# Optimization experiments

Measured on AMD Instinct MI355X. Metric: run time of the kernel, lower is better.

## Reference

```python
import jax, jax.numpy as jnp
import numpy as np

LN_EPS = 1e-5
EPSILON = 1e-8
NUM_ITERS = 3
SLOT_SIZE = 128
NUM_SLOTS = 7
MLP_HIDDEN = 256


def _layernorm(x, g, b):
    m = jnp.mean(x, axis=-1, keepdims=True)
    v = jnp.var(x, axis=-1, keepdims=True)
    return (x - m) * jax.lax.rsqrt(v + LN_EPS) * g + b


def setup_inputs() -> dict:
    key = jax.random.key(0)
    ks = jax.random.split(key, 16)
    B, N, D, S, H, M = 64, 4096, 128, NUM_SLOTS, SLOT_SIZE, MLP_HIDDEN
    sc = 0.05
    return {
        "inputs": jax.random.normal(ks[0], (B, N, D), jnp.float32),
        "slots_init": jax.random.normal(ks[1], (B, S, H + 4), jnp.float32),
        "ln_in_g": jnp.ones((D,), jnp.float32), "ln_in_b": jnp.zeros((D,), jnp.float32),
        "ln_s_g": jnp.ones((H,), jnp.float32), "ln_s_b": jnp.zeros((H,), jnp.float32),
        "ln_m_g": jnp.ones((H,), jnp.float32), "ln_m_b": jnp.zeros((H,), jnp.float32),
        "Wq": jax.random.normal(ks[2], (H, H), jnp.float32) * sc,
        "Wk": jax.random.normal(ks[3], (H, H), jnp.float32) * sc,
        "Wv": jax.random.normal(ks[4], (H, H), jnp.float32) * sc,
        "W_ih": jax.random.normal(ks[5], (3 * H, H), jnp.float32) * sc,
        "W_hh": jax.random.normal(ks[6], (3 * H, H), jnp.float32) * sc,
        "b_ih": jnp.zeros((3 * H,), jnp.float32),
        "b_hh": jnp.zeros((3 * H,), jnp.float32),
        "mlp_w1": jax.random.normal(ks[7], (M, H), jnp.float32) * sc,
        "mlp_b1": jnp.zeros((M,), jnp.float32),
        "mlp_w2": jax.random.normal(ks[8], (H, M), jnp.float32) * sc,
        "mlp_b2": jnp.zeros((H,), jnp.float32),
        "slots_mu": jax.random.normal(ks[9], (1, 1, H + 4), jnp.float32) * sc,
        "slots_log_sigma": jax.random.normal(ks[10], (1, 1, H + 4), jnp.float32) * sc,
    }


def _gru_cell(x, h, W_ih, W_hh, b_ih, b_hh):
    # torch.nn.GRUCell math; x, h: [..., H]
    gi = x @ W_ih.T + b_ih
    gh = h @ W_hh.T + b_hh
    i_r, i_z, i_n = jnp.split(gi, 3, axis=-1)
    h_r, h_z, h_n = jnp.split(gh, 3, axis=-1)
    r = jax.nn.sigmoid(i_r + h_r)
    z = jax.nn.sigmoid(i_z + h_z)
    n = jnp.tanh(i_n + r * h_n)
    return (1.0 - z) * n + z * h


def reference(inputs, slots_init, ln_in_g, ln_in_b, ln_s_g, ln_s_b, ln_m_g, ln_m_b,
              Wq, Wk, Wv, W_ih, W_hh, b_ih, b_hh, mlp_w1, mlp_b1, mlp_w2, mlp_b2,
              slots_mu, slots_log_sigma):
    x = _layernorm(inputs, ln_in_g, ln_in_b)           # [B, N, D]
    k = x @ Wk.T                                       # [B, N, H]
    v = x @ Wv.T                                       # [B, N, H]
    slots_full = slots_mu + jnp.exp(slots_log_sigma) * slots_init  # [B, S, H+4]
    slots = slots_full[..., :SLOT_SIZE]                # positions/scales discarded
    scale = SLOT_SIZE ** -0.5
    for _ in range(NUM_ITERS):
        slots_prev = slots
        sn = _layernorm(slots, ln_s_g, ln_s_b)
        q = sn @ Wq.T                                  # [B, S, H]
        logits = scale * jnp.einsum('bnh,bsh->bns', k, q)
        attn = jax.nn.softmax(logits, axis=-1) + EPSILON
        attn = attn / jnp.sum(attn, axis=1, keepdims=True)
        updates = jnp.einsum('bns,bnh->bsh', attn, v)  # [B, S, H]
        slots = _gru_cell(updates, slots_prev, W_ih, W_hh, b_ih, b_hh)
        slots = slots + (jax.nn.relu(_layernorm(slots, ln_m_g, ln_m_b) @ mlp_w1.T + mlp_b1) @ mlp_w2.T + mlp_b2)
    return slots
```

## Files before the change

kernel.cpp:

```cpp
#include <hip/hip_runtime.h>
#include <hip/hip_bf16.h>
#include <stdint.h>

typedef unsigned int u32;
typedef unsigned short u16;
typedef float v2f __attribute__((ext_vector_type(2)));
typedef short bf16x8 __attribute__((ext_vector_type(8)));
typedef float f32x4 __attribute__((ext_vector_type(4)));

#define LN_EPS_ 1e-5f
#define EPS_ 1e-8f

__device__ __forceinline__ float bflo(u32 v){ return __uint_as_float(v << 16); }
__device__ __forceinline__ float bfhi(u32 v){ return __uint_as_float(v & 0xFFFF0000u); }
__device__ __forceinline__ u32 f2bf(float f){
    u32 x = __float_as_uint(f);
    return (x + 0x7FFFu + ((x >> 16) & 1u)) >> 16;
}
__device__ __forceinline__ u32 pack2bf(float a, float b){
    union { __hip_bfloat162 h; u32 u; } cv;
    cv.h = __float22bfloat162_rn(float2{a, b});
    return cv.u;
}
__device__ __forceinline__ v2f pkfma(v2f a, v2f b, v2f c){
    v2f d; asm("v_pk_fma_f32 %0, %1, %2, %3" : "=v"(d) : "v"(a), "v"(b), "v"(c)); return d;
}
__device__ __forceinline__ v2f pkadd(v2f a, v2f b){
    v2f d; asm("v_pk_add_f32 %0, %1, %2" : "=v"(d) : "v"(a), "v"(b)); return d;
}
__device__ __forceinline__ bf16x8 as_bf16x8(uint4 u){
    union { uint4 a; bf16x8 b; } c; c.a = u; return c.b;
}

__global__ __launch_bounds__(256) void k_pack(
    const float* __restrict__ Wq, const float* __restrict__ Wv,
    const float* __restrict__ Wih, const float* __restrict__ Whh,
    const float* __restrict__ w1, const float* __restrict__ w2,
    float* __restrict__ WqT, u32* __restrict__ Pv, u32* __restrict__ Pih,
    u32* __restrict__ Phh, u32* __restrict__ Pw1, u32* __restrict__ Pw2,
    u32* __restrict__ Rg32)
{
    int i = blockIdx.x * 256 + threadIdx.x;
    if (i < 8192) {
        int dp = i >> 7, o = i & 127;
        Pv[i] = pack2bf(Wv[o * 128 + 2 * dp], Wv[o * 128 + 2 * dp + 1]);
    } else if (i < 32768) {
        int r = i - 8192; int dp = r / 384, j = r - dp * 384;
        Pih[r] = pack2bf(Wih[j * 128 + 2 * dp], Wih[j * 128 + 2 * dp + 1]);
    } else if (i < 57344) {
        int r = i - 32768; int dp = r / 384, j = r - dp * 384;
        Phh[r] = pack2bf(Whh[j * 128 + 2 * dp], Whh[j * 128 + 2 * dp + 1]);
    } else if (i < 73728) {
        int r = i - 57344; int dp = r >> 8, j = r & 255;
        Pw1[r] = pack2bf(w1[j * 128 + 2 * dp], w1[j * 128 + 2 * dp + 1]);
    } else if (i < 90112) {
        int r = i - 73728; int mp = r >> 7, o = r & 127;
        Pw2[r] = pack2bf(w2[o * 256 + 2 * mp], w2[o * 256 + 2 * mp + 1]);
    } else if (i < 106496) {
        int r = i - 90112; int d = r >> 7, o = r & 127;
        WqT[r] = Wq[o * 128 + d];
    } else if (i < 143360) {
        int r = i - 106496; int b = r / 576, rem = r - b * 576;
        Rg32[b * 1024 + 448 + rem] = 0;
    }
}

__global__ __launch_bounds__(256) void k_init_prep(
    const float* __restrict__ slots_init, const float* __restrict__ mu,
    const float* __restrict__ ls, float* __restrict__ slots,
    const float* __restrict__ g_s, const float* __restrict__ b_s,
    const float* __restrict__ WqT, const float* __restrict__ Wk,
    const float* __restrict__ g_in, const float* __restrict__ b_in,
    u16* __restrict__ Rg, float* __restrict__ c1ws, float* __restrict__ c2ws)
{
    __shared__ float snb[128], qb[128], xch[128], red4[4];
    int bs = blockIdx.x, t = threadIdx.x;
    int b = bs / 7, s = bs - b * 7;
    int h = t & 127, half = t >> 7;
    float nv = 0.f;
    if (!half) {
        nv = mu[h] + expf(ls[h]) * slots_init[bs * 132 + h];
        slots[bs * 128 + h] = nv;
    }
    if (!half) {
        float smv = nv, sqv = nv * nv;
        for (int m = 32; m >= 1; m >>= 1) { smv += __shfl_xor(smv, m); sqv += __shfl_xor(sqv, m); }
        if ((t & 63) == 0) { red4[(t >> 6) * 2] = smv; red4[(t >> 6) * 2 + 1] = sqv; }
    }
    __syncthreads();
    float mean = (red4[0] + red4[2]) * (1.0f / 128.0f);
    float var  = (red4[1] + red4[3]) * (1.0f / 128.0f) - mean * mean;
    float rsv = rsqrtf(var + LN_EPS_);
    if (!half) snb[h] = (nv - mean) * rsv * g_s[h] + b_s[h];
    __syncthreads();
    {
        float q0 = 0.f, q1 = 0.f;
        int d0 = half * 64;
        #pragma unroll 4
        for (int d = d0; d < d0 + 64; d += 2) {
            q0 += WqT[d * 128 + h] * snb[d];
            q1 += WqT[(d + 1) * 128 + h] * snb[d + 1];
        }
        if (half) xch[h] = q0 + q1;
        __syncthreads();
        if (!half) qb[h] = q0 + q1 + xch[h];
        __syncthreads();
    }
    float r0 = 0.f, r1 = 0.f;
    int j0 = half * 64;
    #pragma unroll 4
    for (int j = j0; j < j0 + 64; j += 2) {
        r0 += Wk[j * 128 + h] * qb[j];
        r1 += Wk[(j + 1) * 128 + h] * qb[j + 1];
    }
    if (half) xch[h] = r0 + r1;
    __syncthreads();
    if (!half) {
        float r = (r0 + r1 + xch[h]) * 0.08838834764831845f;
        float rt  = g_in[h] * r;
        float c2v = b_in[h] * r;
        Rg[((size_t)b * 16 + s) * 128 + h] = (u16)f2bf(rt);
        float c1p = rt, c2p = c2v;
        for (int m = 32; m >= 1; m >>= 1) { c1p += __shfl_xor(c1p, m); c2p += __shfl_xor(c2p, m); }
        if ((t & 63) == 0) { red4[(t >> 6) * 2] = c1p; red4[(t >> 6) * 2 + 1] = c2p; }
    }
    __syncthreads();
    if (t == 0) {
        c1ws[b * 8 + s] = red4[0] + red4[2];
        c2ws[b * 8 + s] = red4[1] + red4[3];
    }
}

__global__ __launch_bounds__(256, 8) void k_attn(
    const float* __restrict__ xin,
    const u16* __restrict__ Rg, const float* __restrict__ c1ws,
    const float* __restrict__ c2ws,
    float* __restrict__ ypart, float* __restrict__ Zp, float* __restrict__ Ap)
{
    __shared__ u32 tile[4096];
    __shared__ __align__(16) float wt[448];
    __shared__ __align__(8)  float stats[128];
    __shared__ float c1l[16], c2l[16];
    __shared__ float redp[4][8], redw[4][8];
    int t = threadIdx.x;
    int b = blockIdx.y;
    int n0 = blockIdx.x * 64;
    int lane = t & 63, wv = t >> 6;
    int ls = lane & 15, lg = lane >> 4;
    size_t blk = (size_t)b * 64 + blockIdx.x;

    if (t < 16) {
        c1l[t] = (t < 7) ? c1ws[b * 8 + t] : 0.f;
        c2l[t] = (t < 7) ? c2ws[b * 8 + t] : 0.f;
    }

    bf16x8 bfr[4];
    {
        const u16* Rrow = Rg + ((size_t)b * 16 + ls) * 128;
        #pragma unroll
        for (int kk = 0; kk < 4; kk++)
            bfr[kk] = as_bf16x8(*(const uint4*)&Rrow[kk * 32 + lg * 8]);
    }

    {
        int r = t >> 2, p = t & 3;
        const float4* xg = (const float4*)(xin + ((size_t)b * 4096 + n0 + r) * 128 + p * 32);
        v2f smp = (v2f){0.f, 0.f}, sqp = (v2f){0.f, 0.f};
        #pragma unroll
        for (int i = 0; i < 8; i++) {
            float4 v = xg[i];
            v2f lo = (v2f){v.x, v.y}, hi = (v2f){v.z, v.w};
            smp = pkadd(smp, pkadd(lo, hi));
            sqp = pkfma(lo, lo, sqp);
            sqp = pkfma(hi, hi, sqp);
            int q = p * 4 + (i >> 1), rem = (i & 1) * 2;
            *(uint2*)&tile[(r * 16 + (q ^ (r & 15))) * 4 + rem] =
                make_uint2(pack2bf(v.x, v.y), pack2bf(v.z, v.w));
        }
        float sm = smp.x + smp.y, sq = sqp.x + sqp.y;
        sm += __shfl_xor(sm, 1); sq += __shfl_xor(sq, 1);
        sm += __shfl_xor(sm, 2); sq += __shfl_xor(sq, 2);
        if (!p) {
            float mean = sm * (1.0f / 128.0f);
            float var  = sq * (1.0f / 128.0f) - mean * mean;
            *(float2*)&stats[2 * r] = make_float2(mean, rsqrtf(var + LN_EPS_));
        }
    }
    __syncthreads();

    f32x4 acc0 = {0.f, 0.f, 0.f, 0.f};
    {
        int m0 = wv * 16 + ls;
        #pragma unroll
        for (int kk = 0; kk < 4; kk++) {
            int q = kk * 4 + lg;
            bf16x8 a0 = as_bf16x8(*(const uint4*)&tile[(m0 * 16 + (q ^ ls)) * 4]);
            acc0 = __builtin_amdgcn_mfma_f32_16x16x32_bf16(a0, bfr[kk], acc0, 0, 0, 0);
        }
    }
    {
        float zsum = 0.f, asum = 0.f;
        float c1v = c1l[ls], c2v = c2l[ls];
        bool sv = ls < 7;
        int nbase = wv * 16 + lg * 4;
        #pragma unroll
        for (int r4 = 0; r4 < 4; r4++) {
            int n = nbase + r4;
            float2 stf = *(const float2*)&stats[2 * n];
            float L = sv ? (stf.y * (acc0[r4] - stf.x * c1v) + c2v) : -3.4e38f;
            float mx = L;
            mx = fmaxf(mx, __shfl_xor(mx, 1));
            mx = fmaxf(mx, __shfl_xor(mx, 2));
            mx = fmaxf(mx, __shfl_xor(mx, 4));
            mx = fmaxf(mx, __shfl_xor(mx, 8));
            float e = __expf(L - mx);
            float ssum = e;
            ssum += __shfl_xor(ssum, 1);
            ssum += __shfl_xor(ssum, 2);
            ssum += __shfl_xor(ssum, 4);
            ssum += __shfl_xor(ssum, 8);
            float p = e * (1.0f / ssum) + EPS_;
            float w = p * stf.y;
            if (sv) {
                wt[ls * 64 + n] = w;
                zsum += p;
                asum += w * stf.x;
            }
        }
        zsum += __shfl_xor(zsum, 16); zsum += __shfl_xor(zsum, 32);
        asum += __shfl_xor(asum, 16); asum += __shfl_xor(asum, 32);
        if (lane < 7) { redp[wv][lane] = zsum; redw[wv][lane] = asum; }
    }
    __syncthreads();
    if (t < 7)
        Zp[blk * 8 + t] = redp[0][t] + redp[1][t] + redp[2][t] + redp[3][t];
    else if (t >= 64 && t < 71) {
        int s = t - 64;
        Ap[blk * 8 + s] = redw[0][s] + redw[1][s] + redw[2][s] + redw[3][s];
    }

    int nh = t >> 7, dp = t & 63, sA = (t >> 6) & 1;
    v2f aclo[4], achi[4];
    #pragma unroll
    for (int k = 0; k < 4; k++) { aclo[k] = (v2f){0.f,0.f}; achi[k] = (v2f){0.f,0.f}; }
    int nbeg = nh * 32;
    #pragma unroll 4
    for (int n = nbeg; n < nbeg + 32; n += 2) {
        u32 x0 = tile[(n * 16 + ((dp >> 2) ^ (n & 15))) * 4 + (dp & 3)];
        u32 x1 = tile[((n + 1) * 16 + ((dp >> 2) ^ ((n + 1) & 15))) * 4 + (dp & 3)];
        v2f alo = (v2f){bflo(x0), bflo(x1)};
        v2f ahi = (v2f){bfhi(x0), bfhi(x1)};
        #pragma unroll
        for (int k = 0; k < 4; k++) {
            int s = sA + 2 * k;
            if (s < 7) {
                v2f wp = *(const v2f*)&wt[s * 64 + n];
                aclo[k] = pkfma(alo, wp, aclo[k]);
                achi[k] = pkfma(ahi, wp, achi[k]);
            }
        }
    }
    float* ytmp = (float*)tile;
    __syncthreads();
    if (nh) {
        #pragma unroll
        for (int k = 0; k < 4; k++) {
            int s = sA + 2 * k;
            if (s < 7)
                *(float2*)&ytmp[s * 128 + 2 * dp] =
                    make_float2(aclo[k].x + aclo[k].y, achi[k].x + achi[k].y);
        }
    }
    __syncthreads();
    if (!nh) {
        float* yp = ypart + blk * 896;
        #pragma unroll
        for (int k = 0; k < 4; k++) {
            int s = sA + 2 * k;
            if (s < 7) {
                float2 o = *(const float2*)&ytmp[s * 128 + 2 * dp];
                *(float2*)&yp[s * 128 + 2 * dp] =
                    make_float2(aclo[k].x + aclo[k].y + o.x,
                                achi[k].x + achi[k].y + o.y);
            }
        }
    }
}

__global__ __launch_bounds__(512) void k_update(
    float* __restrict__ slots, const float* __restrict__ ypart,
    const float* __restrict__ Zp, const float* __restrict__ Ap,
    const float* __restrict__ g_in, const float* __restrict__ b_in,
    const u32* __restrict__ Pv, const u32* __restrict__ Pih,
    const u32* __restrict__ Phh, const float* __restrict__ b_ih,
    const float* __restrict__ b_hh, const float* __restrict__ g_m,
    const float* __restrict__ b_m, const u32* __restrict__ Pw1,
    const float* __restrict__ bb1, const u32* __restrict__ Pw2,
    const float* __restrict__ bb2, float* __restrict__ out,
    const float* __restrict__ g_s, const float* __restrict__ b_s,
    const float* __restrict__ WqT, const float* __restrict__ Wk,
    u16* __restrict__ Rg, float* __restrict__ c1ws, float* __restrict__ c2ws,
    int do_prep)
{
    __shared__ float ybuf[128], ub[128], hb[128], lb[128], t1b[256];
    __shared__ float red4w[4][128];
    __shared__ float g6[12][128];
    __shared__ float m1p[256];
    __shared__ float redA[2], redB[2];
    __shared__ float snb[128], qb[128], red4[4];
    __shared__ float Zsh, Ash;
    int bs = blockIdx.x, t = threadIdx.x;
    int b = bs / 7, s = bs - b * 7;
    int h = t & 127, q = t >> 7;
    {
        float ysum = 0.f;
        const float* bp = ypart + ((size_t)(b * 64 + q * 16)) * 896 + s * 128 + h;
        #pragma unroll 8
        for (int c = 0; c < 16; c++) ysum += bp[(size_t)c * 896];
        red4w[q][h] = ysum;
    }
    if (t < 64) {
        float z = Zp[((size_t)b * 64 + t) * 8 + s];
        for (int m = 32; m >= 1; m >>= 1) z += __shfl_xor(z, m);
        if (t == 0) Zsh = z;
    } else if (t < 128) {
        float a_ = Ap[((size_t)b * 64 + (t - 64)) * 8 + s];
        for (int m = 32; m >= 1; m >>= 1) a_ += __shfl_xor(a_, m);
        if (t == 64) Ash = a_;
    }
    __syncthreads();
    if (q == 0) {
        float ytot = red4w[0][h] + red4w[1][h] + red4w[2][h] + red4w[3][h];
        ybuf[h] = g_in[h] * (ytot - Ash) / Zsh + b_in[h];
        hb[h] = slots[bs * 128 + h];
    }
    __syncthreads();
    {
        float a0 = 0.f;
        int dp0 = q * 16;
        #pragma unroll 4
        for (int dp = dp0; dp < dp0 + 16; dp++) {
            u32 w0 = Pv[dp * 128 + h];
            a0 += bflo(w0) * ybuf[2 * dp] + bfhi(w0) * ybuf[2 * dp + 1];
        }
        red4w[q][h] = a0;
    }
    __syncthreads();
    if (q == 0) ub[h] = red4w[0][h] + red4w[1][h] + red4w[2][h] + red4w[3][h];
    __syncthreads();
    {
        const u32* P = (q >= 2) ? Phh : Pih;
        const float* src = (q >= 2) ? hb : ub;
        int dp0 = (q & 1) * 32;
        float gv0 = 0.f, gv1 = 0.f, gv2 = 0.f;
        #pragma unroll 4
        for (int dp = dp0; dp < dp0 + 32; dp++) {
            float x0 = src[2 * dp], x1 = src[2 * dp + 1];
            u32 w0 = P[dp * 384 + h];
            u32 w1v = P[dp * 384 + 128 + h];
            u32 w2v = P[dp * 384 + 256 + h];
            gv0 += bflo(w0) * x0 + bfhi(w0) * x1;
            gv1 += bflo(w1v) * x0 + bfhi(w1v) * x1;
            gv2 += bflo(w2v) * x0 + bfhi(w2v) * x1;
        }
        g6[q * 3 + 0][h] = gv0; g6[q * 3 + 1][h] = gv1; g6[q * 3 + 2][h] = gv2;
    }
    __syncthreads();
    float hv = 0.f;
    if (q == 0) {
        float gi0 = g6[0][h] + g6[3][h] + b_ih[h];
        float gi1 = g6[1][h] + g6[4][h] + b_ih[128 + h];
        float gi2 = g6[2][h] + g6[5][h] + b_ih[256 + h];
        float gh0 = g6[6][h] + g6[9][h]  + b_hh[h];
        float gh1 = g6[7][h] + g6[10][h] + b_hh[128 + h];
        float gh2 = g6[8][h] + g6[11][h] + b_hh[256 + h];
        float rg = 1.0f / (1.0f + __expf(-(gi0 + gh0)));
        float zg = 1.0f / (1.0f + __expf(-(gi1 + gh1)));
        float ng = tanhf(gi2 + rg * gh2);
        hv = (1.0f - zg) * ng + zg * hb[h];
        float sm2 = hv, sq2 = hv * hv;
        for (int m = 32; m >= 1; m >>= 1) { sm2 += __shfl_xor(sm2, m); sq2 += __shfl_xor(sq2, m); }
        if ((t & 63) == 0) { redA[t >> 6] = sm2; redB[t >> 6] = sq2; }
    }
    __syncthreads();
    if (q == 0) {
        float sm2 = redA[0] + redA[1], sq2 = redB[0] + redB[1];
        float mean = sm2 * (1.0f / 128.0f);
        float var  = sq2 * (1.0f / 128.0f) - mean * mean;
        float rsq = rsqrtf(var + LN_EPS_);
        lb[h] = (hv - mean) * rsq * g_m[h] + b_m[h];
    }
    __syncthreads();
    {
        int o = t & 255, kh = t >> 8;
        float m1 = 0.f;
        int dp0 = kh * 32;
        #pragma unroll 4
        for (int dp = dp0; dp < dp0 + 32; dp++) {
            u32 w0 = Pw1[dp * 256 + o];
            m1 += bflo(w0) * lb[2 * dp] + bfhi(w0) * lb[2 * dp + 1];
        }
        if (kh) m1p[o] = m1;
        __syncthreads();
        if (!kh) t1b[o] = fmaxf(m1 + m1p[o] + bb1[o], 0.0f);
    }
    __syncthreads();
    {
        float o0 = 0.f;
        int mp0 = q * 32;
        #pragma unroll 4
        for (int mp = mp0; mp < mp0 + 32; mp++) {
            u32 w0 = Pw2[mp * 128 + h];
            o0 += bflo(w0) * t1b[2 * mp] + bfhi(w0) * t1b[2 * mp + 1];
        }
        red4w[q][h] = o0;
    }
    __syncthreads();
    float nv = 0.f;
    if (q == 0) {
        nv = hv + bb2[h] + red4w[0][h] + red4w[1][h] + red4w[2][h] + red4w[3][h];
        slots[bs * 128 + h] = nv;
        out[bs * 128 + h] = nv;
    }
    if (do_prep) {
        __syncthreads();
        if (q == 0) {
            float smv = nv, sqv = nv * nv;
            for (int m = 32; m >= 1; m >>= 1) { smv += __shfl_xor(smv, m); sqv += __shfl_xor(sqv, m); }
            if ((t & 63) == 0) { red4[(t >> 6) * 2] = smv; red4[(t >> 6) * 2 + 1] = sqv; }
        }
        __syncthreads();
        float mean = (red4[0] + red4[2]) * (1.0f / 128.0f);
        float var  = (red4[1] + red4[3]) * (1.0f / 128.0f) - mean * mean;
        float rsv = rsqrtf(var + LN_EPS_);
        if (q == 0) snb[h] = (nv - mean) * rsv * g_s[h] + b_s[h];
        __syncthreads();
        {
            float qv = 0.f;
            int d0 = q * 32;
            #pragma unroll 4
            for (int d = d0; d < d0 + 32; d++) qv += WqT[d * 128 + h] * snb[d];
            red4w[q][h] = qv;
        }
        __syncthreads();
        if (q == 0) qb[h] = red4w[0][h] + red4w[1][h] + red4w[2][h] + red4w[3][h];
        __syncthreads();
        {
            float rv = 0.f;
            int j0 = q * 32;
            #pragma unroll 4
            for (int j = j0; j < j0 + 32; j++) rv += Wk[j * 128 + h] * qb[j];
            red4w[q][h] = rv;
        }
        __syncthreads();
        if (q == 0) {
            float r = (red4w[0][h] + red4w[1][h] + red4w[2][h] + red4w[3][h])
                      * 0.08838834764831845f;
            float rt  = g_in[h] * r;
            float c2v = b_in[h] * r;
            Rg[((size_t)b * 16 + s) * 128 + h] = (u16)f2bf(rt);
            float c1p = rt, c2p = c2v;
            for (int m = 32; m >= 1; m >>= 1) { c1p += __shfl_xor(c1p, m); c2p += __shfl_xor(c2p, m); }
            if ((t & 63) == 0) { red4[(t >> 6) * 2] = c1p; red4[(t >> 6) * 2 + 1] = c2p; }
        }
        __syncthreads();
        if (t == 0) {
            c1ws[b * 8 + s] = red4[0] + red4[2];
            c2ws[b * 8 + s] = red4[1] + red4[3];
        }
    }
}

extern "C" void kernel_launch(void* const* d_in, const int* in_sizes, int n_in,
                              void* d_out, int out_size, void* d_ws, size_t ws_size,
                              hipStream_t stream) {
    const float* inputs     = (const float*)d_in[0];
    const float* slots_init = (const float*)d_in[1];
    const float* ln_in_g    = (const float*)d_in[2];
    const float* ln_in_b    = (const float*)d_in[3];
    const float* ln_s_g     = (const float*)d_in[4];
    const float* ln_s_b     = (const float*)d_in[5];
    const float* ln_m_g     = (const float*)d_in[6];
    const float* ln_m_b     = (const float*)d_in[7];
    const float* Wq         = (const float*)d_in[8];
    const float* Wk         = (const float*)d_in[9];
    const float* Wv         = (const float*)d_in[10];
    const float* W_ih       = (const float*)d_in[11];
    const float* W_hh       = (const float*)d_in[12];
    const float* b_ih       = (const float*)d_in[13];
    const float* b_hh       = (const float*)d_in[14];
    const float* mlp_w1     = (const float*)d_in[15];
    const float* mlp_b1     = (const float*)d_in[16];
    const float* mlp_w2     = (const float*)d_in[17];
    const float* mlp_b2     = (const float*)d_in[18];
    const float* slots_mu   = (const float*)d_in[19];
    const float* slots_ls   = (const float*)d_in[20];

    char* ws = (char*)d_ws;
    float* slots = (float*)(ws);
    u16*   Rg    = (u16*)  (ws + 229376);
    float* c1ws  = (float*)(ws + 491520);
    float* c2ws  = (float*)(ws + 493568);
    float* WqT   = (float*)(ws + 495616);
    u32*   Pv    = (u32*)  (ws + 561152);
    u32*   Pih   = (u32*)  (ws + 593920);
    u32*   Phh   = (u32*)  (ws + 692224);
    u32*   Pw1   = (u32*)  (ws + 790528);
    u32*   Pw2   = (u32*)  (ws + 856064);
    float* Zp    = (float*)(ws + 921600);
    float* Ap    = (float*)(ws + 1052672);
    float* ypart = (float*)(ws + 1183744);

    k_pack<<<560, 256, 0, stream>>>(Wq, Wv, W_ih, W_hh, mlp_w1, mlp_w2,
                                    WqT, Pv, Pih, Phh, Pw1, Pw2, (u32*)Rg);
    k_init_prep<<<448, 256, 0, stream>>>(slots_init, slots_mu, slots_ls, slots,
                                         ln_s_g, ln_s_b, WqT, Wk, ln_in_g, ln_in_b,
                                         Rg, c1ws, c2ws);
    for (int it = 0; it < 3; it++) {
        k_attn<<<dim3(64, 64), 256, 0, stream>>>(inputs, Rg, c1ws, c2ws,
                                                 ypart, Zp, Ap);
        k_update<<<448, 512, 0, stream>>>(slots, ypart, Zp, Ap, ln_in_g, ln_in_b,
                                          Pv, Pih, Phh, b_ih, b_hh,
                                          ln_m_g, ln_m_b, Pw1, mlp_b1, Pw2, mlp_b2,
                                          (float*)d_out,
                                          ln_s_g, ln_s_b, WqT, Wk,
                                          Rg, c1ws, c2ws, (it < 2) ? 1 : 0);
    }
}
```

Before: 368.8 us.

## Compute attention-weighted value accumulation with bf16 MFMA instead of packed FMA

The per-block weighted sum of input rows over attention weights (attn^T x) moves from scalar packed-FP32 FMAs to 16x16x32 bf16 MFMA instructions. Attention weights are packed to bf16 in shared memory and gathered into the MFMA operand layout, and the input tile is repacked into B fragments. This drops the cross-half reduction through shared memory and its two barriers. In exchange the weights are rounded to bf16, which costs some precision, and the gather does some bit shuffling of the tile reads.

```diff
diff --git a/kernel.cpp b/kernel.cpp
--- a/kernel.cpp
+++ b/kernel.cpp
@@ -138,8 +138,8 @@
     float* __restrict__ ypart, float* __restrict__ Zp, float* __restrict__ Ap)
 {
     __shared__ u32 tile[4096];
-    __shared__ __align__(16) float wt[448];
-    __shared__ __align__(8)  float stats[128];
+    __shared__ u32 wtp[16 * 36];
+    __shared__ __align__(8) float stats[128];
     __shared__ float c1l[16], c2l[16];
     __shared__ float redp[4][8], redw[4][8];
     int t = threadIdx.x;
@@ -203,6 +203,7 @@
         float c1v = c1l[ls], c2v = c2l[ls];
         bool sv = ls < 7;
         int nbase = wv * 16 + lg * 4;
+        float wv4[4];
         #pragma unroll
         for (int r4 = 0; r4 < 4; r4++) {
             int n = nbase + r4;
@@ -221,12 +222,14 @@
             ssum += __shfl_xor(ssum, 8);
             float p = e * (1.0f / ssum) + EPS_;
             float w = p * stf.y;
+            wv4[r4] = w;
             if (sv) {
-                wt[ls * 64 + n] = w;
                 zsum += p;
                 asum += w * stf.x;
             }
         }
+        wtp[ls * 36 + wv * 8 + lg * 2 + 0] = pack2bf(wv4[0], wv4[1]);
+        wtp[ls * 36 + wv * 8 + lg * 2 + 1] = pack2bf(wv4[2], wv4[3]);
         zsum += __shfl_xor(zsum, 16); zsum += __shfl_xor(zsum, 32);
         asum += __shfl_xor(asum, 16); asum += __shfl_xor(asum, 32);
         if (lane < 7) { redp[wv][lane] = zsum; redw[wv][lane] = asum; }
@@ -239,50 +242,42 @@
         Ap[blk * 8 + s] = redw[0][s] + redw[1][s] + redw[2][s] + redw[3][s];
     }
 
-    int nh = t >> 7, dp = t & 63, sA = (t >> 6) & 1;
-    v2f aclo[4], achi[4];
+    bf16x8 af0 = as_bf16x8(*(const uint4*)&wtp[ls * 36 + lg * 4]);
+    bf16x8 af1 = as_bf16x8(*(const uint4*)&wtp[ls * 36 + 16 + lg * 4]);
+    float* yp = ypart + blk * 896;
+    u32 selhi = ls & 1;
     #pragma unroll
-    for (int k = 0; k < 4; k++) { aclo[k] = (v2f){0.f,0.f}; achi[k] = (v2f){0.f,0.f}; }
-    int nbeg = nh * 32;
-    #pragma unroll 4
-    for (int n = nbeg; n < nbeg + 32; n += 2) {
-        u32 x0 = tile[(n * 16 + ((dp >> 2) ^ (n & 15))) * 4 + (dp & 3)];
-        u32 x1 = tile[((n + 1) * 16 + ((dp >> 2) ^ ((n + 1) & 15))) * 4 + (dp & 3)];
-        v2f alo = (v2f){bflo(x0), bflo(x1)};
-        v2f ahi = (v2f){bfhi(x0), bfhi(x1)};
+    for (int hs = 0; hs < 2; hs++) {
+        int hsub = wv * 2 + hs;
+        int dp = hsub * 8 + (ls >> 1);
+        int qc = dp >> 2, rem = dp & 3;
+        f32x4 acc2 = {0.f, 0.f, 0.f, 0.f};
         #pragma unroll
-        for (int k = 0; k < 4; k++) {
-            int s = sA + 2 * k;
-            if (s < 7) {
-                v2f wp = *(const v2f*)&wt[s * 64 + n];
-                aclo[k] = pkfma(alo, wp, aclo[k]);
-                achi[k] = pkfma(ahi, wp, achi[k]);
+        for (int ks = 0; ks < 2; ks++) {
+            u32 xr[8];
+            #pragma unroll
+            for (int i = 0; i < 8; i++) {
+                int n = ks * 32 + lg * 8 + i;
+                xr[i] = tile[(n * 16 + (qc ^ (n & 15))) * 4 + rem];
             }
-        }
-    }
-    float* ytmp = (float*)tile;
-    __syncthreads();
-    if (nh) {
+            u32 bw[4];
+            #pragma unroll
+            for (int j = 0; j < 4; j++) {
+                u32 a = xr[2 * j], c = xr[2 * j + 1];
+                u32 lo16 = selhi ? (a >> 16) : (a & 0xFFFFu);
+                u32 hi16 = selhi ? (c & 0xFFFF0000u) : (c << 16);
+                bw[j] = lo16 | hi16;
+            }
+            acc2 = __builtin_amdgcn_mfma_f32_16x16x32_bf16(
+                ks ? af1 : af0,
+                as_bf16x8(make_uint4(bw[0], bw[1], bw[2], bw[3])),
+                acc2, 0, 0, 0);
+        }
+        int h = hsub * 16 + ls;
         #pragma unroll
-        for (int k = 0; k < 4; k++) {
-            int s = sA + 2 * k;
-            if (s < 7)
-                *(float2*)&ytmp[s * 128 + 2 * dp] =
-                    make_float2(aclo[k].x + aclo[k].y, achi[k].x + achi[k].y);
-        }
-    }
-    __syncthreads();
-    if (!nh) {
-        float* yp = ypart + blk * 896;
-        #pragma unroll
-        for (int k = 0; k < 4; k++) {
-            int s = sA + 2 * k;
-            if (s < 7) {
-                float2 o = *(const float2*)&ytmp[s * 128 + 2 * dp];
-                *(float2*)&yp[s * 128 + 2 * dp] =
-                    make_float2(aclo[k].x + aclo[k].y + o.x,
-                                achi[k].x + achi[k].y + o.y);
-            }
+        for (int r = 0; r < 4; r++) {
+            int s = lg * 4 + r;
+            if (s < 7) yp[s * 128 + h] = acc2[r];
         }
     }
 }
```

New measurement: 363.1 us. Within noise of the previous version (-1.6%).
